# Kernel tuning notes

Hardware: AMD Instinct MI355X
Metric: run time of the kernel (lower is better)

Reference implementation:

```python
import jax, jax.numpy as jnp
import numpy as np

B, STREAM, IN_CH = 128, 512, 4
EXTRA, GROUPS, DEPTH = 5, 2, 3
STEP, LENGTH = 16, 32
RNN, OUT = 256, 10
C = IN_CH + 1 + EXTRA              # augmented channels: original + time + 1x1-conv
SIG_C = C + C * C + C ** 3          # signature channels per group at depth 3
W = (STREAM - LENGTH) // STEP + 1   # number of sliding windows = GRU steps
F = GROUPS * SIG_C                  # GRU input features


def _outer(a, b):
    # flattened tensor (outer) product on last axis: (...,m),(...,n)->(...,m*n)
    return (a[..., :, None] * b[..., None, :]).reshape(a.shape[:-1] + (a.shape[-1] * b.shape[-1],))


def _chen_step(S, dx):
    # Chen's identity: S <- S (tensor) exp(dx). S is a tuple of flattened
    # signature levels (..., C^k), k=1..DEPTH; dx has shape (..., C).
    P = [jnp.ones(dx.shape[:-1] + (1,), dx.dtype)]  # dx^{(x)j}/j!, j=0..DEPTH
    for j in range(1, DEPTH + 1):
        P.append(_outer(P[-1], dx) / j)
    newS = []
    for k in range(1, DEPTH + 1):
        acc = P[k]  # S_0 (x) P_k
        for j in range(k):
            acc = acc + _outer(S[k - 1 - j], P[j])
        newS.append(acc)
    return tuple(newS)


def setup_inputs() -> dict:
    key = jax.random.key(0)
    ks = jax.random.split(key, 10)
    s_aug = 1.0 / np.sqrt(IN_CH)
    s_rnn = 1.0 / np.sqrt(RNN)
    return {
        "x": jax.random.normal(ks[0], (B, STREAM, IN_CH), jnp.float32),
        "W_aug": jax.random.uniform(ks[1], (GROUPS, EXTRA, IN_CH), jnp.float32, -s_aug, s_aug),
        "b_aug": jax.random.uniform(ks[2], (GROUPS, EXTRA), jnp.float32, -s_aug, s_aug),
        "W_ih": jax.random.uniform(ks[3], (3 * RNN, F), jnp.float32, -s_rnn, s_rnn),
        "W_hh": jax.random.uniform(ks[4], (3 * RNN, RNN), jnp.float32, -s_rnn, s_rnn),
        "b_ih": jax.random.uniform(ks[5], (3 * RNN,), jnp.float32, -s_rnn, s_rnn),
        "b_hh": jax.random.uniform(ks[6], (3 * RNN,), jnp.float32, -s_rnn, s_rnn),
        "W_out": jax.random.uniform(ks[7], (OUT, RNN), jnp.float32, -s_rnn, s_rnn),
        "b_out": jax.random.uniform(ks[8], (OUT,), jnp.float32, -s_rnn, s_rnn),
    }


def reference(x, W_aug, b_aug, W_ih, W_hh, b_ih, b_hh, W_out, b_out):
    # (a) linear augmentation per channel group: [original | time | conv1x1(x)]
    t = jnp.linspace(0.0, 1.0, STREAM, dtype=x.dtype)
    t = jnp.broadcast_to(t[None, :, None], (B, STREAM, 1))
    aug = jnp.einsum('bsi,gei->bgse', x, W_aug) + b_aug[None, :, None, :]  # (B,G,S,EXTRA)
    base = jnp.broadcast_to(jnp.concatenate([x, t], -1)[:, None],
                            (B, GROUPS, STREAM, IN_CH + 1))
    xa = jnp.concatenate([base, aug], -1)            # (B,G,S,C)
    xa = xa.reshape(B * GROUPS, STREAM, C)

    # (b) depth-3 signatures over sliding windows via Chen's identity
    dx = xa[:, 1:] - xa[:, :-1]                       # (BG, S-1, C)
    widx = jnp.arange(W)[:, None] * STEP + jnp.arange(LENGTH - 1)[None, :]
    dxw = dx[:, widx]                                 # (BG, W, L-1, C)
    dxw = jnp.moveaxis(dxw, 2, 0)                     # (L-1, BG, W, C)
    S0 = tuple(jnp.zeros((B * GROUPS, W, C ** k), x.dtype) for k in range(1, DEPTH + 1))
    S, _ = jax.lax.scan(lambda S, d: (_chen_step(S, d), None), S0, dxw)
    sig = jnp.concatenate(S, -1)                      # (BG, W, SIG_C)
    sig = sig.reshape(B, GROUPS, W, SIG_C)
    sig = jnp.moveaxis(sig, 2, 0).reshape(W, B, F)    # (W, B, G*SIG_C)

    # (c) GRU over window signatures (torch.nn.GRUCell math, gate order r,z,n)
    def gru(h, xt):
        gi = xt @ W_ih.T + b_ih
        gh = h @ W_hh.T + b_hh
        ir, iz, inn = jnp.split(gi, 3, -1)
        hr, hz, hn = jnp.split(gh, 3, -1)
        r = jax.nn.sigmoid(ir + hr)
        z = jax.nn.sigmoid(iz + hz)
        n = jnp.tanh(inn + r * hn)
        return (1 - z) * n + z * h, None

    h, _ = jax.lax.scan(gru, jnp.zeros((B, RNN), x.dtype), sig)
    return jax.nn.sigmoid(h @ W_out.T + b_out)        # (B, OUT)
```

## Files before the change

### kernel.cpp

```cpp
#include <hip/hip_runtime.h>
#include <hip/hip_bf16.h>
#include <stdint.h>


typedef _Float16 f16;
typedef f16  f16x4 __attribute__((ext_vector_type(4)));
typedef f16  f16x8 __attribute__((ext_vector_type(8)));
typedef float f32x2 __attribute__((ext_vector_type(2)));
typedef float f32x4 __attribute__((ext_vector_type(4)));

#define ASYNC16(gp, lp) __builtin_amdgcn_global_load_lds( \
    (const __attribute__((address_space(1))) void*)(gp),  \
    (__attribute__((address_space(3))) void*)(lp), 16, 0, 0)

#define BAR_LDS() do { asm volatile("s_waitcnt lgkmcnt(0)" ::: "memory"); \
                       __builtin_amdgcn_s_barrier();                      \
                       asm volatile("" ::: "memory"); } while (0)

__device__ __forceinline__ float fexp2(float x) {
    float r; asm("v_exp_f32 %0, %1" : "=v"(r) : "v"(x)); return r;
}
__device__ __forceinline__ float frcp(float x) {
    float r; asm("v_rcp_f32 %0, %1" : "=v"(r) : "v"(x)); return r;
}

__global__ __launch_bounds__(256) void prep_kernel(const float* __restrict__ x,
                                                   const float* __restrict__ W_aug,
                                                   const float* __restrict__ Wih,
                                                   const float* __restrict__ Whh,
                                                   f16* __restrict__ sig16,
                                                   f16* __restrict__ wih16,
                                                   f16* __restrict__ whh16,
                                                   uint8_t* __restrict__ whh8) {
    __shared__ float dxs[4][31][10];
    const int tid = threadIdx.x;
    if (blockIdx.x < 840) {
        int c = blockIdx.x * 256 + tid;
        int r = c / 280, kc = (c - r * 280) * 8;
        const float* src = Wih + (size_t)r * 2220 + kc;
        f16x8 o;
        if (kc + 8 <= 2220) {
            float4 v0 = *(const float4*)(src);
            float4 v1 = *(const float4*)(src + 4);
            o[0]=(f16)v0.x; o[1]=(f16)v0.y; o[2]=(f16)v0.z; o[3]=(f16)v0.w;
            o[4]=(f16)v1.x; o[5]=(f16)v1.y; o[6]=(f16)v1.z; o[7]=(f16)v1.w;
        } else {
#pragma unroll
            for (int j = 0; j < 8; j++)
                o[j] = (f16)((kc + j < 2220) ? src[j] : 0.0f);
        }
        *(f16x8*)(wih16 + (size_t)r * 2240 + kc) = o;
        return;
    }
    if (blockIdx.x < 936) {
        int c2 = ((int)blockIdx.x - 840) * 256 + tid;
        int j8 = c2 * 8;
        float w[8];
        {
            float4 v0 = *(const float4*)(Whh + j8);
            float4 v1 = *(const float4*)(Whh + j8 + 4);
            w[0]=v0.x; w[1]=v0.y; w[2]=v0.z; w[3]=v0.w;
            w[4]=v1.x; w[5]=v1.y; w[6]=v1.z; w[7]=v1.w;
        }
        f16x8 o;
#pragma unroll
        for (int j = 0; j < 8; j++) o[j] = (f16)w[j];
        *(f16x8*)(whh16 + j8) = o;
        if (j8 < 131072) {
            uint32_t p01 = (uint32_t)__builtin_amdgcn_cvt_pk_fp8_f32(w[0]*16.f, w[1]*16.f, 0, false) & 0xffffu;
            uint32_t p23 = (uint32_t)__builtin_amdgcn_cvt_pk_fp8_f32(w[2]*16.f, w[3]*16.f, 0, false) & 0xffffu;
            uint32_t p45 = (uint32_t)__builtin_amdgcn_cvt_pk_fp8_f32(w[4]*16.f, w[5]*16.f, 0, false) & 0xffffu;
            uint32_t p67 = (uint32_t)__builtin_amdgcn_cvt_pk_fp8_f32(w[6]*16.f, w[7]*16.f, 0, false) & 0xffffu;
            uint2 st = make_uint2(p01 | (p23 << 16), p45 | (p67 << 16));
            *(uint2*)(whh8 + j8) = st;
        }
        return;
    }
    const int sub = tid >> 6, t64 = tid & 63;
    const int cid = ((int)blockIdx.x - 936) * 4 + sub;
    const int w = cid % 31;
    const int bg = cid / 31;
    const int b = bg >> 1, g = bg & 1;
    if (t64 < 31) {
        int s = w * 16 + t64;
        const float4 x0 = *(const float4*)(x + ((size_t)b * 512 + s) * 4);
        const float4 x1 = *(const float4*)(x + ((size_t)b * 512 + s + 1) * 4);
        float d0 = x1.x - x0.x, d1 = x1.y - x0.y, d2 = x1.z - x0.z, d3 = x1.w - x0.w;
        dxs[sub][t64][0] = d0; dxs[sub][t64][1] = d1;
        dxs[sub][t64][2] = d2; dxs[sub][t64][3] = d3;
        dxs[sub][t64][4] = 1.0f / 511.0f;
#pragma unroll
        for (int e = 0; e < 5; e++) {
            const float* wa = W_aug + (g * 5 + e) * 4;
            dxs[sub][t64][5 + e] = d0 * wa[0] + d1 * wa[1] + d2 * wa[2] + d3 * wa[3];
        }
    }
    __syncthreads();
    size_t base = ((size_t)(w * 128 + b)) * 2240 + (size_t)g * 1110;
    if (t64 < 50) {
        int p0 = 2 * t64, p1 = p0 + 1;
        int i0 = p0 / 10, j0 = p0 % 10, j1 = j0 + 1;
        const float* dz  = &dxs[sub][0][0];
        const float* pI  = dz + i0;
        const float* pJ0 = dz + j0;
        const float* pJ1 = dz + j1;
        float s3a[10], s3b[10];
#pragma unroll
        for (int k = 0; k < 10; k++) { s3a[k] = 0.f; s3b[k] = 0.f; }
        float s2a = 0.f, s2b = 0.f, s1 = 0.f;
        for (int l = 0; l < 31; l++) {
            const float* row = dz + l * 10;
            float di  = pI[l * 10];
            float dj0 = pJ0[l * 10];
            float dj1 = pJ1[l * 10];
            float t0 = s1 + di * (1.0f / 3.0f);
            float a0 = s2a + t0 * (0.5f * dj0);
            float a1 = s2b + t0 * (0.5f * dj1);
#pragma unroll
            for (int k = 0; k < 10; k++) {
                float dk = row[k];
                s3a[k] += a0 * dk;
                s3b[k] += a1 * dk;
            }
            float u = s1 + 0.5f * di;
            s2a += u * dj0;
            s2b += u * dj1;
            s1 += di;
        }
        sig16[base + 10 + p0] = (f16)s2a;
        sig16[base + 10 + p1] = (f16)s2b;
#pragma unroll
        for (int k = 0; k < 10; k++) {
            sig16[base + 110 + p0 * 10 + k] = (f16)s3a[k];
            sig16[base + 110 + p1 * 10 + k] = (f16)s3b[k];
        }
    } else if (t64 < 60) {
        int c = t64 - 50;
        const float* pc = &dxs[sub][0][0] + c;
        float s = 0.f;
        for (int l = 0; l < 31; l++) s += pc[l * 10];
        sig16[base + c] = (f16)s;
    }
    if (g == 1 && t64 < 20)
        sig16[((size_t)(w * 128 + b)) * 2240 + 2220 + t64] = (f16)0.0f;
}

__global__ __launch_bounds__(256) void gemm_kernel(const f16* __restrict__ A,
                                                   const f16* __restrict__ Bw,
                                                   const float* __restrict__ bias,
                                                   const float* __restrict__ bhh,
                                                   f16* __restrict__ Cgi) {
    const int lin = blockIdx.x;
    const int t = (lin & 7) + 8 * (lin / 48);
    const int nb = (lin >> 3) % 6;
    if (t >= 31) return;
    __shared__ __align__(16) f16 As[7][128 * 32];
    __shared__ __align__(16) f16 Bs[7][128 * 32];
    const int tid = threadIdx.x, lane = tid & 63, wid = tid >> 6;
    const int wm = wid >> 1, wn = wid & 1;
    const int Mbase = t * 128, Nbase = nb * 128;
    const int lr = lane >> 2, lk = lane & 3;
    const int l16 = lane & 15, quad = lane >> 4;
    const int r0a = wid * 32, r0b = wid * 32 + 16;
    const f16* gaA0 = A  + (size_t)(Mbase + r0a + lr) * 2240 + lk * 8;
    const f16* gaA1 = A  + (size_t)(Mbase + r0b + lr) * 2240 + lk * 8;
    const f16* gbB0 = Bw + (size_t)(Nbase + r0a + lr) * 2240 + lk * 8;
    const f16* gbB1 = Bw + (size_t)(Nbase + r0b + lr) * 2240 + lk * 8;

#define GISSUE(KT, BUF) do { \
        int _k0 = (KT) * 32; \
        ASYNC16(gaA0 + _k0, &As[BUF][r0a * 32]); \
        ASYNC16(gbB0 + _k0, &Bs[BUF][r0a * 32]); \
        ASYNC16(gaA1 + _k0, &As[BUF][r0b * 32]); \
        ASYNC16(gbB1 + _k0, &Bs[BUF][r0b * 32]); } while (0)

#define GCOMPUTE(BUF) do { \
        f16x8 af[4], bf[4]; \
        _Pragma("unroll") \
        for (int mt = 0; mt < 4; mt++) \
            af[mt] = *(const f16x8*)&As[BUF][(wm * 64 + mt * 16 + l16) * 32 + quad * 8]; \
        _Pragma("unroll") \
        for (int nt = 0; nt < 4; nt++) \
            bf[nt] = *(const f16x8*)&Bs[BUF][(wn * 64 + nt * 16 + l16) * 32 + quad * 8]; \
        _Pragma("unroll") \
        for (int mt = 0; mt < 4; mt++) \
            _Pragma("unroll") \
            for (int nt = 0; nt < 4; nt++) \
                acc[mt][nt] = __builtin_amdgcn_mfma_f32_16x16x32_f16(af[mt], bf[nt], acc[mt][nt], 0, 0, 0); } while (0)

    f32x4 acc[4][4];
#pragma unroll
    for (int mt = 0; mt < 4; mt++)
#pragma unroll
        for (int nt = 0; nt < 4; nt++) acc[mt][nt] = (f32x4){0.f, 0.f, 0.f, 0.f};

    GISSUE(0, 0); GISSUE(1, 1); GISSUE(2, 2);
    GISSUE(3, 3); GISSUE(4, 4); GISSUE(5, 5);
    for (int kt = 0; kt < 64; kt++) {
        asm volatile("s_waitcnt vmcnt(20) lgkmcnt(0)\n\ts_barrier" ::: "memory");
        GISSUE(kt + 6, (kt + 6) % 7);
        GCOMPUTE(kt % 7);
    }
    asm volatile("s_waitcnt vmcnt(0) lgkmcnt(0)\n\ts_barrier" ::: "memory");
    GCOMPUTE(64 % 7); GCOMPUTE(65 % 7); GCOMPUTE(66 % 7);
    GCOMPUTE(67 % 7); GCOMPUTE(68 % 7); GCOMPUTE(69 % 7);

    const float NEG_LOG2E = -1.4426950408889634f;
    const float TWO_LOG2E =  2.8853900817779268f;
#pragma unroll
    for (int mt = 0; mt < 4; mt++) {
        const int bbv = wm * 4 + mt;
#pragma unroll
        for (int nt = 0; nt < 4; nt++) {
            int col = Nbase + wn * 64 + nt * 16 + l16;
            float bvv = bias[col] + (col < 512 ? bhh[col] : 0.0f);
            float scl = (col < 512) ? NEG_LOG2E : TWO_LOG2E;
            int gs = col >> 8, hcc = col & 255;
            int gw = hcc >> 5, gtc = (hcc >> 4) & 1, gl = hcc & 15;
            int u = gs * 2 + gtc;
            int gtid = gw * 64 + quad * 16 + gl;
            size_t off = ((size_t)((t * 8 + bbv) * 6 + u)) * 2048 + (size_t)gtid * 4;
            f16x4 st;
#pragma unroll
            for (int rr = 0; rr < 4; rr++) st[rr] = (f16)((acc[mt][nt][rr] + bvv) * scl);
            *(f16x4*)(Cgi + off) = st;
        }
    }
#undef GISSUE
#undef GCOMPUTE
}

#define ACLOB \
  "a0","a1","a2","a3","a4","a5","a6","a7","a8","a9","a10","a11","a12","a13","a14","a15", \
  "a16","a17","a18","a19","a20","a21","a22","a23","a24","a25","a26","a27","a28","a29","a30","a31", \
  "a32","a33","a34","a35","a36","a37","a38","a39","a40","a41","a42","a43","a44","a45","a46","a47", \
  "a48","a49","a50","a51","a52","a53","a54","a55","a56","a57","a58","a59","a60","a61","a62","a63", \
  "a64","a65","a66","a67","a68","a69","a70","a71","a72","a73","a74","a75","a76","a77","a78","a79", \
  "a80","a81","a82","a83","a84","a85","a86","a87","a88","a89","a90","a91","a92","a93","a94","a95", \
  "a96","a97","a98","a99","a100","a101","a102","a103","a104","a105","a106","a107","a108","a109","a110","a111", \
  "a112","a113","a114","a115","a116","a117","a118","a119","a120","a121","a122","a123","a124","a125","a126","a127"

#define LF8(A0,A1, U, KT) do { \
  f32x2 _t = *(const f32x2*)(whh8 + (size_t)(((U) >> 1) * 256 + wid * 32 + ((U) & 1) * 16 + l16) * 256 + (KT) * 32 + quad * 8); \
  asm volatile("v_accvgpr_write_b32 a" #A0 ", %0\n\t" \
               "v_accvgpr_write_b32 a" #A1 ", %1" \
               :: "v"(_t[0]), "v"(_t[1]) : "a" #A0, "a" #A1); } while (0)

#define LFN(A0,A1,A2,A3, TC, KT) do { \
  f32x4 _t = *(const f32x4*)(whh16 + (size_t)(512 + wid * 32 + (TC) * 16 + l16) * 256 + (KT) * 32 + quad * 8); \
  asm volatile("v_accvgpr_write_b32 a" #A0 ", %0\n\t" \
               "v_accvgpr_write_b32 a" #A1 ", %1\n\t" \
               "v_accvgpr_write_b32 a" #A2 ", %2\n\t" \
               "v_accvgpr_write_b32 a" #A3 ", %3" \
               :: "v"(_t[0]), "v"(_t[1]), "v"(_t[2]), "v"(_t[3]) \
               : "a" #A0, "a" #A1, "a" #A2, "a" #A3); } while (0)

#define FP8GZ(P, F0,F1,F2,F3) \
  "v_mfma_f32_16x16x32_fp8_fp8 %[aR0], " P ", a[" F0 "], %[zq]\n\t" \
  "v_mfma_f32_16x16x32_fp8_fp8 %[aR1], " P ", a[" F1 "], %[zq]\n\t" \
  "v_mfma_f32_16x16x32_fp8_fp8 %[aZ0], " P ", a[" F2 "], %[zq]\n\t" \
  "v_mfma_f32_16x16x32_fp8_fp8 %[aZ1], " P ", a[" F3 "], %[zq]\n\t"

#define FP8G(P, F0,F1,F2,F3) \
  "v_mfma_f32_16x16x32_fp8_fp8 %[aR0], " P ", a[" F0 "], %[aR0]\n\t" \
  "v_mfma_f32_16x16x32_fp8_fp8 %[aR1], " P ", a[" F1 "], %[aR1]\n\t" \
  "v_mfma_f32_16x16x32_fp8_fp8 %[aZ0], " P ", a[" F2 "], %[aZ0]\n\t" \
  "v_mfma_f32_16x16x32_fp8_fp8 %[aZ1], " P ", a[" F3 "], %[aZ1]\n\t"

#define F16GZ(Q, G0,G1) \
  "v_mfma_f32_16x16x32_f16 %[aN0], " Q ", a[" G0 "], %[zq]\n\t" \
  "v_mfma_f32_16x16x32_f16 %[aN1], " Q ", a[" G1 "], %[zq]\n\t"

#define F16G(Q, G0,G1) \
  "v_mfma_f32_16x16x32_f16 %[aN0], " Q ", a[" G0 "], %[aN0]\n\t" \
  "v_mfma_f32_16x16x32_f16 %[aN1], " Q ", a[" G1 "], %[aN1]\n\t"

__global__ __launch_bounds__(512, 2) void gru_kernel(const f16* __restrict__ gi,
                                                     const f16* __restrict__ whh16,
                                                     const uint8_t* __restrict__ whh8,
                                                     const float* __restrict__ b_hh,
                                                     const float* __restrict__ W_out,
                                                     const float* __restrict__ b_out,
                                                     float* __restrict__ out) {
    __shared__ __align__(16) f16 hbufF[2][16 * 280];
    __shared__ __align__(16) uint8_t hbuf8[2][16 * 272];
    const int tid = threadIdx.x, lane = tid & 63, wid = tid >> 6;
    const int quad = lane >> 4, l16 = lane & 15;
    const int bb = blockIdx.x;

    for (int i = tid; i < 16 * 280; i += 512) hbufF[1][i] = (f16)0.0f;
    for (int i = tid; i < 16 * 272; i += 512) hbuf8[1][i] = 0;

    LF8(0,1, 0,0);   LF8(2,3, 0,1);   LF8(4,5, 0,2);   LF8(6,7, 0,3);
    LF8(8,9, 0,4);   LF8(10,11, 0,5); LF8(12,13, 0,6); LF8(14,15, 0,7);
    LF8(16,17, 1,0); LF8(18,19, 1,1); LF8(20,21, 1,2); LF8(22,23, 1,3);
    LF8(24,25, 1,4); LF8(26,27, 1,5); LF8(28,29, 1,6); LF8(30,31, 1,7);
    LF8(32,33, 2,0); LF8(34,35, 2,1); LF8(36,37, 2,2); LF8(38,39, 2,3);
    LF8(40,41, 2,4); LF8(42,43, 2,5); LF8(44,45, 2,6); LF8(46,47, 2,7);
    LF8(48,49, 3,0); LF8(50,51, 3,1); LF8(52,53, 3,2); LF8(54,55, 3,3);
    LF8(56,57, 3,4); LF8(58,59, 3,5); LF8(60,61, 3,6); LF8(62,63, 3,7);
    LFN(64,65,66,67,   0,0); LFN(68,69,70,71,   0,1); LFN(72,73,74,75,   0,2); LFN(76,77,78,79,   0,3);
    LFN(80,81,82,83,   0,4); LFN(84,85,86,87,   0,5); LFN(88,89,90,91,   0,6); LFN(92,93,94,95,   0,7);
    LFN(96,97,98,99,   1,0); LFN(100,101,102,103, 1,1); LFN(104,105,106,107, 1,2); LFN(108,109,110,111, 1,3);
    LFN(112,113,114,115, 1,4); LFN(116,117,118,119, 1,5); LFN(120,121,122,123, 1,6); LFN(124,125,126,127, 1,7);

    const float C2 = 2.8853900817779268f;
    float bhn[2];
#pragma unroll
    for (int tc = 0; tc < 2; tc++) bhn[tc] = C2 * b_hh[512 + wid * 32 + tc * 16 + l16];
    float hm[2][4];
#pragma unroll
    for (int tc = 0; tc < 2; tc++)
#pragma unroll
        for (int rr = 0; rr < 4; rr++) hm[tc][rr] = 0.f;

    uint32_t aF0 = (uint32_t)(uintptr_t)(__attribute__((address_space(3))) const void*)
                       (&hbufF[0][l16 * 280 + quad * 8]);
    uint32_t aF1 = (uint32_t)(uintptr_t)(__attribute__((address_space(3))) const void*)
                       (&hbufF[1][l16 * 280 + quad * 8]);
    uint32_t a80 = (uint32_t)(uintptr_t)(__attribute__((address_space(3))) const void*)
                       (&hbuf8[0][l16 * 272 + quad * 8]);
    uint32_t a81 = (uint32_t)(uintptr_t)(__attribute__((address_space(3))) const void*)
                       (&hbuf8[1][l16 * 272 + quad * 8]);

    const size_t lanebase = (size_t)bb * 12288 + (size_t)tid * 4;
    f16x4 gcur[6];
#pragma unroll
    for (int u = 0; u < 6; u++)
        gcur[u] = *(const f16x4*)(gi + lanebase + u * 2048);

    const f32x4 zq = (f32x4){0.f, 0.f, 0.f, 0.f};

    BAR_LDS();

    for (int t = 0; t < 31; t++) {
        const uint32_t a8 = (t & 1) ? a80 : a81;
        const uint32_t aF = (t & 1) ? aF0 : aF1;
        f32x4 aR0, aR1, aZ0, aZ1, aN0, aN1;
        f32x2 p0, p1, p2;
        f32x4 q0, q1, q2;
        asm volatile(
            "s_setprio 1\n\t"
            "ds_read_b64  %[p0], %[a8] offset:0\n\t"
            "ds_read_b128 %[q0], %[aF] offset:0\n\t"
            "ds_read_b64  %[p1], %[a8] offset:32\n\t"
            "ds_read_b128 %[q1], %[aF] offset:64\n\t"
            "ds_read_b64  %[p2], %[a8] offset:64\n\t"
            "ds_read_b128 %[q2], %[aF] offset:128\n\t"
            "s_waitcnt lgkmcnt(5)\n\t"
            FP8GZ("%[p0]", "0:1","16:17","32:33","48:49")
            "ds_read_b64  %[p0], %[a8] offset:96\n\t"
            "s_waitcnt lgkmcnt(5)\n\t"
            F16GZ("%[q0]", "64:67","96:99")
            "ds_read_b128 %[q0], %[aF] offset:192\n\t"
            "s_waitcnt lgkmcnt(5)\n\t"
            FP8G("%[p1]", "2:3","18:19","34:35","50:51")
            "ds_read_b64  %[p1], %[a8] offset:128\n\t"
            "s_waitcnt lgkmcnt(5)\n\t"
            F16G("%[q1]", "68:71","100:103")
            "ds_read_b128 %[q1], %[aF] offset:256\n\t"
            "s_waitcnt lgkmcnt(5)\n\t"
            FP8G("%[p2]", "4:5","20:21","36:37","52:53")
            "ds_read_b64  %[p2], %[a8] offset:160\n\t"
            "s_waitcnt lgkmcnt(5)\n\t"
            F16G("%[q2]", "72:75","104:107")
            "ds_read_b128 %[q2], %[aF] offset:320\n\t"
            "s_waitcnt lgkmcnt(5)\n\t"
            FP8G("%[p0]", "6:7","22:23","38:39","54:55")
            "ds_read_b64  %[p0], %[a8] offset:192\n\t"
            "s_waitcnt lgkmcnt(5)\n\t"
            F16G("%[q0]", "76:79","108:111")
            "ds_read_b128 %[q0], %[aF] offset:384\n\t"
            "s_waitcnt lgkmcnt(5)\n\t"
            FP8G("%[p1]", "8:9","24:25","40:41","56:57")
            "ds_read_b64  %[p1], %[a8] offset:224\n\t"
            "s_waitcnt lgkmcnt(5)\n\t"
            F16G("%[q1]", "80:83","112:115")
            "ds_read_b128 %[q1], %[aF] offset:448\n\t"
            "s_waitcnt lgkmcnt(5)\n\t"
            FP8G("%[p2]", "10:11","26:27","42:43","58:59")
            "s_waitcnt lgkmcnt(4)\n\t"
            F16G("%[q2]", "84:87","116:119")
            "s_waitcnt lgkmcnt(3)\n\t"
            FP8G("%[p0]", "12:13","28:29","44:45","60:61")
            "s_waitcnt lgkmcnt(2)\n\t"
            F16G("%[q0]", "88:91","120:123")
            "s_waitcnt lgkmcnt(1)\n\t"
            FP8G("%[p1]", "14:15","30:31","46:47","62:63")
            "s_waitcnt lgkmcnt(0)\n\t"
            F16G("%[q1]", "92:95","124:127")
            "s_setprio 0\n\t"
            "s_nop 7\n\ts_nop 7"
            : [aR0]"=&v"(aR0), [aR1]"=&v"(aR1), [aZ0]"=&v"(aZ0), [aZ1]"=&v"(aZ1),
              [aN0]"=&v"(aN0), [aN1]"=&v"(aN1),
              [p0]"=&v"(p0), [p1]"=&v"(p1), [p2]"=&v"(p2),
              [q0]"=&v"(q0), [q1]"=&v"(q1), [q2]"=&v"(q2)
            : [a8]"v"(a8), [aF]"v"(aF), [zq]"v"(zq)
            : ACLOB);

        f16* hdF = hbufF[t & 1];
        uint8_t* hd8 = hbuf8[t & 1];
        const float C1N16 = -0.09016844005556021f;
#pragma unroll
        for (int tc = 0; tc < 2; tc++) {
            const int hcx = wid * 32 + tc * 16 + l16;
            const f32x4 vR = tc ? aR1 : aR0;
            const f32x4 vZ = tc ? aZ1 : aZ0;
            const f32x4 vN = tc ? aN1 : aN0;
#pragma unroll
            for (int rr = 0; rr < 4; rr++) {
                float rg = frcp(1.f + fexp2(fmaf(C1N16, vR[rr], (float)gcur[tc][rr])));
                float zg = frcp(1.f + fexp2(fmaf(C1N16, vZ[rr], (float)gcur[2 + tc][rr])));
                float t2 = fmaf(rg, fmaf(C2, vN[rr], bhn[tc]), (float)gcur[4 + tc][rr]);
                float e2 = fexp2(t2);
                float ng = fmaf(-2.f, frcp(e2 + 1.f), 1.f);
                float h  = fmaf(zg, hm[tc][rr] - ng, ng);
                hm[tc][rr] = h;
                hdF[(quad * 4 + rr) * 280 + hcx] = (f16)h;
                int pk = __builtin_amdgcn_cvt_pk_fp8_f32(h, h, 0, false);
                hd8[(quad * 4 + rr) * 272 + hcx] = (uint8_t)pk;
            }
        }
        {
            int tn = (t < 30) ? t + 1 : 30;
            const f16* gsrc = gi + (size_t)tn * 98304 + lanebase;
#pragma unroll
            for (int u = 0; u < 6; u++)
                gcur[u] = *(const f16x4*)(gsrc + u * 2048);
        }
        BAR_LDS();
    }
    if (tid < 160) {
        int r = tid / 10, oc = tid - r * 10;
        const f16* hfin = hbufF[0];
        float s = b_out[oc];
        for (int k = 0; k < 256; k++) s += (float)hfin[r * 280 + k] * W_out[oc * 256 + k];
        out[(bb * 16 + r) * 10 + oc] = frcp(1.f + __expf(-s));
    }
}

extern "C" void kernel_launch(void* const* d_in, const int* in_sizes, int n_in,
                              void* d_out, int out_size, void* d_ws, size_t ws_size,
                              hipStream_t stream) {
    const float* x     = (const float*)d_in[0];
    const float* W_aug = (const float*)d_in[1];
    const float* W_ih  = (const float*)d_in[3];
    const float* W_hh  = (const float*)d_in[4];
    const float* b_ih  = (const float*)d_in[5];
    const float* b_hh  = (const float*)d_in[6];
    const float* W_out = (const float*)d_in[7];
    const float* b_out = (const float*)d_in[8];
    float* out = (float*)d_out;

    char* ws = (char*)d_ws;
    const size_t SIG_BYTES  = (size_t)3968 * 2240 * 2;
    const size_t WIH_BYTES  = (size_t)768 * 2240 * 2;
    const size_t WHH_BYTES  = (size_t)768 * 256 * 2;
    const size_t WHH8_BYTES = (size_t)512 * 256;
    const size_t GI_BYTES   = (size_t)31 * 8 * 6 * 512 * 4 * 2;
    if (ws_size < SIG_BYTES + WIH_BYTES + WHH_BYTES + WHH8_BYTES + GI_BYTES) return;
    f16* sig16    = (f16*)ws;
    f16* wih16    = (f16*)(ws + SIG_BYTES);
    f16* whh16    = (f16*)(ws + SIG_BYTES + WIH_BYTES);
    uint8_t* whh8 = (uint8_t*)(ws + SIG_BYTES + WIH_BYTES + WHH_BYTES);
    f16* giw      = (f16*)(ws + SIG_BYTES + WIH_BYTES + WHH_BYTES + WHH8_BYTES);

    hipLaunchKernelGGL(prep_kernel, dim3(2920), dim3(256), 0, stream,
                       x, W_aug, W_ih, W_hh, sig16, wih16, whh16, whh8);
    hipLaunchKernelGGL(gemm_kernel, dim3(192), dim3(256), 0, stream,
                       sig16, wih16, b_ih, b_hh, giw);
    hipLaunchKernelGGL(gru_kernel, dim3(8), dim3(512), 0, stream,
                       giw, whh16, whh8, b_hh, W_out, b_out, out);
}
```

Before: 212.4 us.

## Use 8 waves per GEMM block and pack signature stores as half2

The input-projection GEMM block now runs 512 threads (8 waves) instead of 256. Each wave owns a 64x32 output sub-tile and issues one A and one B async row-load per k-step, and the vmcnt wait threshold is lowered to match. The goal is more latency hiding and MFMA issue per CU, since only 186 blocks are active. In the signature prep kernel, fp16 stores of level-2/3 terms and the padding zeros are packed into 2-wide vector stores to cut store instruction count. The larger block adds register pressure and uses the same LDS footprint.

```diff
diff --git a/kernel.cpp b/kernel.cpp
--- a/kernel.cpp
+++ b/kernel.cpp
@@ -4,6 +4,7 @@
 
 
 typedef _Float16 f16;
+typedef f16  f16x2 __attribute__((ext_vector_type(2)));
 typedef f16  f16x4 __attribute__((ext_vector_type(4)));
 typedef f16  f16x8 __attribute__((ext_vector_type(8)));
 typedef float f32x2 __attribute__((ext_vector_type(2)));
@@ -127,13 +128,15 @@
             s2b += u * dj1;
             s1 += di;
         }
-        sig16[base + 10 + p0] = (f16)s2a;
-        sig16[base + 10 + p1] = (f16)s2b;
-#pragma unroll
-        for (int k = 0; k < 10; k++) {
-            sig16[base + 110 + p0 * 10 + k] = (f16)s3a[k];
-            sig16[base + 110 + p1 * 10 + k] = (f16)s3b[k];
-        }
+        *(f16x2*)(sig16 + base + 10 + p0) = (f16x2){(f16)s2a, (f16)s2b};
+#pragma unroll
+        for (int k = 0; k < 5; k++)
+            *(f16x2*)(sig16 + base + 110 + p0 * 10 + 2 * k) =
+                (f16x2){(f16)s3a[2 * k], (f16)s3a[2 * k + 1]};
+#pragma unroll
+        for (int k = 0; k < 5; k++)
+            *(f16x2*)(sig16 + base + 110 + p1 * 10 + 2 * k) =
+                (f16x2){(f16)s3b[2 * k], (f16)s3b[2 * k + 1]};
     } else if (t64 < 60) {
         int c = t64 - 50;
         const float* pc = &dxs[sub][0][0] + c;
@@ -141,11 +144,12 @@
         for (int l = 0; l < 31; l++) s += pc[l * 10];
         sig16[base + c] = (f16)s;
     }
-    if (g == 1 && t64 < 20)
-        sig16[((size_t)(w * 128 + b)) * 2240 + 2220 + t64] = (f16)0.0f;
-}
-
-__global__ __launch_bounds__(256) void gemm_kernel(const f16* __restrict__ A,
+    if (g == 1 && t64 < 10)
+        *(f16x2*)(sig16 + ((size_t)(w * 128 + b)) * 2240 + 2220 + 2 * t64) =
+            (f16x2){(f16)0.0f, (f16)0.0f};
+}
+
+__global__ __launch_bounds__(512) void gemm_kernel(const f16* __restrict__ A,
                                                    const f16* __restrict__ Bw,
                                                    const float* __restrict__ bias,
                                                    const float* __restrict__ bhh,
@@ -157,53 +161,49 @@
     __shared__ __align__(16) f16 As[7][128 * 32];
     __shared__ __align__(16) f16 Bs[7][128 * 32];
     const int tid = threadIdx.x, lane = tid & 63, wid = tid >> 6;
-    const int wm = wid >> 1, wn = wid & 1;
+    const int wm = wid >> 2, wn = wid & 3;
     const int Mbase = t * 128, Nbase = nb * 128;
     const int lr = lane >> 2, lk = lane & 3;
     const int l16 = lane & 15, quad = lane >> 4;
-    const int r0a = wid * 32, r0b = wid * 32 + 16;
-    const f16* gaA0 = A  + (size_t)(Mbase + r0a + lr) * 2240 + lk * 8;
-    const f16* gaA1 = A  + (size_t)(Mbase + r0b + lr) * 2240 + lk * 8;
-    const f16* gbB0 = Bw + (size_t)(Nbase + r0a + lr) * 2240 + lk * 8;
-    const f16* gbB1 = Bw + (size_t)(Nbase + r0b + lr) * 2240 + lk * 8;
+    const int r0 = wid * 16;
+    const f16* gaA0 = A  + (size_t)(Mbase + r0 + lr) * 2240 + lk * 8;
+    const f16* gbB0 = Bw + (size_t)(Nbase + r0 + lr) * 2240 + lk * 8;
 
 #define GISSUE(KT, BUF) do { \
         int _k0 = (KT) * 32; \
-        ASYNC16(gaA0 + _k0, &As[BUF][r0a * 32]); \
-        ASYNC16(gbB0 + _k0, &Bs[BUF][r0a * 32]); \
-        ASYNC16(gaA1 + _k0, &As[BUF][r0b * 32]); \
-        ASYNC16(gbB1 + _k0, &Bs[BUF][r0b * 32]); } while (0)
+        ASYNC16(gaA0 + _k0, &As[BUF][r0 * 32]); \
+        ASYNC16(gbB0 + _k0, &Bs[BUF][r0 * 32]); } while (0)
 
 #define GCOMPUTE(BUF) do { \
-        f16x8 af[4], bf[4]; \
+        f16x8 af[4], bf[2]; \
         _Pragma("unroll") \
         for (int mt = 0; mt < 4; mt++) \
             af[mt] = *(const f16x8*)&As[BUF][(wm * 64 + mt * 16 + l16) * 32 + quad * 8]; \
         _Pragma("unroll") \
-        for (int nt = 0; nt < 4; nt++) \
-            bf[nt] = *(const f16x8*)&Bs[BUF][(wn * 64 + nt * 16 + l16) * 32 + quad * 8]; \
+        for (int nt = 0; nt < 2; nt++) \
+            bf[nt] = *(const f16x8*)&Bs[BUF][(wn * 32 + nt * 16 + l16) * 32 + quad * 8]; \
         _Pragma("unroll") \
         for (int mt = 0; mt < 4; mt++) \
             _Pragma("unroll") \
-            for (int nt = 0; nt < 4; nt++) \
+            for (int nt = 0; nt < 2; nt++) \
                 acc[mt][nt] = __builtin_amdgcn_mfma_f32_16x16x32_f16(af[mt], bf[nt], acc[mt][nt], 0, 0, 0); } while (0)
 
-    f32x4 acc[4][4];
+    f32x4 acc[4][2];
 #pragma unroll
     for (int mt = 0; mt < 4; mt++)
 #pragma unroll
-        for (int nt = 0; nt < 4; nt++) acc[mt][nt] = (f32x4){0.f, 0.f, 0.f, 0.f};
+        for (int nt = 0; nt < 2; nt++) acc[mt][nt] = (f32x4){0.f, 0.f, 0.f, 0.f};
 
     GISSUE(0, 0); GISSUE(1, 1); GISSUE(2, 2);
     GISSUE(3, 3); GISSUE(4, 4); GISSUE(5, 5);
     for (int kt = 0; kt < 64; kt++) {
-        asm volatile("s_waitcnt vmcnt(20) lgkmcnt(0)\n\ts_barrier" ::: "memory");
+        asm volatile("s_waitcnt vmcnt(10) lgkmcnt(0)\n\ts_barrier" ::: "memory");
         GISSUE(kt + 6, (kt + 6) % 7);
         GCOMPUTE(kt % 7);
     }
     asm volatile("s_waitcnt vmcnt(0) lgkmcnt(0)\n\ts_barrier" ::: "memory");
-    GCOMPUTE(64 % 7); GCOMPUTE(65 % 7); GCOMPUTE(66 % 7);
-    GCOMPUTE(67 % 7); GCOMPUTE(68 % 7); GCOMPUTE(69 % 7);
+    GCOMPUTE(1); GCOMPUTE(2); GCOMPUTE(3);
+    GCOMPUTE(4); GCOMPUTE(5); GCOMPUTE(6);
 
     const float NEG_LOG2E = -1.4426950408889634f;
     const float TWO_LOG2E =  2.8853900817779268f;
@@ -211,8 +211,8 @@
     for (int mt = 0; mt < 4; mt++) {
         const int bbv = wm * 4 + mt;
 #pragma unroll
-        for (int nt = 0; nt < 4; nt++) {
-            int col = Nbase + wn * 64 + nt * 16 + l16;
+        for (int nt = 0; nt < 2; nt++) {
+            int col = Nbase + wn * 32 + nt * 16 + l16;
             float bvv = bias[col] + (col < 512 ? bhh[col] : 0.0f);
             float scl = (col < 512) ? NEG_LOG2E : TWO_LOG2E;
             int gs = col >> 8, hcc = col & 255;
@@ -467,7 +467,7 @@
 
     hipLaunchKernelGGL(prep_kernel, dim3(2920), dim3(256), 0, stream,
                        x, W_aug, W_ih, W_hh, sig16, wih16, whh16, whh8);
-    hipLaunchKernelGGL(gemm_kernel, dim3(192), dim3(256), 0, stream,
+    hipLaunchKernelGGL(gemm_kernel, dim3(192), dim3(512), 0, stream,
                        sig16, wih16, b_ih, b_hh, giw);
     hipLaunchKernelGGL(gru_kernel, dim3(8), dim3(512), 0, stream,
                        giw, whh16, whh8, b_hh, W_out, b_out, out);
```

Result: faster. 200.0 us (-5.8%).
